# Kernel tuning notes

Measured on AMD Instinct MI355X. Metric: run time of the kernel, lower is better.

Reference implementation:

```python
import jax, jax.numpy as jnp
import numpy as np

HIDDEN, NH, NKV, HD = 2048, 16, 2, 128
CTX, NL, POS = 4096, 36, 3000
THETA, EPS = 1.0e6, 1e-6


def _rope_cos_sin(pos):
    inv_freq = 1.0 / (THETA ** (jnp.arange(0, HD, 2, dtype=jnp.float32) / HD))  # [HD/2]
    ang = pos * inv_freq
    ang = jnp.concatenate([ang, ang])  # [HD]
    return jnp.cos(ang), jnp.sin(ang)


def _rotate_half(x):
    x1, x2 = x[..., : HD // 2], x[..., HD // 2 :]
    return jnp.concatenate([-x2, x1], axis=-1)


def setup_inputs() -> dict:
    key = jax.random.key(0)
    ks = jax.random.split(key, 12)
    w = lambda k, shape, s=0.02: (jax.random.normal(k, shape, dtype=jnp.float32) * s)
    mask = jnp.where(jnp.arange(CTX) <= POS, 0.0, -1e9).astype(jnp.float32).reshape(1, 1, 1, CTX)
    return {
        "hidden_states": jax.random.normal(ks[0], (1, 1, HIDDEN), dtype=jnp.float32),
        "position_ids": jnp.array([POS], dtype=jnp.int64 if jax.config.jax_enable_x64 else jnp.int32),
        "causal_mask": mask,
        "current_pos": POS,
        "ln_w": jnp.ones((HIDDEN,), jnp.float32) + w(ks[1], (HIDDEN,)),
        "wq": w(ks[2], (NH * HD, HIDDEN)),
        "bq": w(ks[3], (NH * HD,)),
        "wk": w(ks[4], (NKV * HD, HIDDEN)),
        "bk": w(ks[5], (NKV * HD,)),
        "wv": w(ks[6], (NKV * HD, HIDDEN)),
        "bv": w(ks[7], (NKV * HD,)),
        "wo": w(ks[8], (HIDDEN, NH * HD)),
        "kv_cache": w(ks[9], (2 * NL, NKV, CTX, HD), 1.0),
    }


def reference(hidden_states, position_ids, causal_mask, current_pos,
              ln_w, wq, bq, wk, bk, wv, bv, wo, kv_cache):
    x = hidden_states  # [1,1,H]
    # RMSNorm
    var = jnp.mean(x * x, axis=-1, keepdims=True)
    nx = x * jax.lax.rsqrt(var + EPS) * ln_w

    # QKV projections (single token)
    t = nx[0, 0]  # [H]
    q = (wq @ t + bq).reshape(NH, HD)    # [NH, HD]
    k = (wk @ t + bk).reshape(NKV, HD)   # [NKV, HD]
    v = (wv @ t + bv).reshape(NKV, HD)

    # RoPE at current position
    cos, sin = _rope_cos_sin(jnp.float32(current_pos))
    q = q * cos + _rotate_half(q) * sin
    k = k * cos + _rotate_half(k) * sin

    # KV-cache scatter write: key at layer slot 0, value at slot NL
    kv_cache = kv_cache.at[0, :, current_pos, :].set(k)
    kv_cache = kv_cache.at[NL, :, current_pos, :].set(v)
    key_cache = kv_cache[0]    # [NKV, CTX, HD]
    value_cache = kv_cache[NL]

    # GQA attention over full cache
    rep = NH // NKV
    K = jnp.repeat(key_cache, rep, axis=0)    # [NH, CTX, HD]
    V = jnp.repeat(value_cache, rep, axis=0)
    scores = jnp.einsum("hd,hkd->hk", q, K) / jnp.sqrt(jnp.float32(HD))
    scores = scores + causal_mask[0, 0, 0]    # [NH, CTX]
    probs = jax.nn.softmax(scores, axis=-1)
    ctx = jnp.einsum("hk,hkd->hd", probs, V)  # [NH, HD]
    attn_out = (wo @ ctx.reshape(NH * HD)).reshape(1, 1, HIDDEN)

    return hidden_states + attn_out
```

## Files before the change

### kernel.cpp

```cpp
#include <hip/hip_runtime.h>
#include <hip/hip_bf16.h>
#include <math.h>

#define HIDDEN 2048
#define NH 16
#define NKV 2
#define HD 128
#define CTX 4096
#define NL 36
#define EPS 1e-6f

#define CHUNK 128
#define NCHUNKS (CTX / CHUNK)
#define HPB 4
#define NGRP (NH / HPB)

#define WS_QRAW 0
#define WS_KRAW 2048
#define WS_VRAW 2304
#define WS_TAB  2560
#define WS_PML  2688
#define WS_PACC 3712

#define RSQRT_HD 0.08838834764831845f

__device__ __forceinline__ float dot4(float4 a, float4 b) {
    return a.x*b.x + a.y*b.y + a.z*b.z + a.w*b.w;
}

__global__ __launch_bounds__(256, 1) void qkv_kernel(
    const float* __restrict__ x, const float* __restrict__ lnw,
    const float* __restrict__ wq, const float* __restrict__ bq,
    const float* __restrict__ wk, const float* __restrict__ bk,
    const float* __restrict__ wv, const float* __restrict__ bv,
    const int* __restrict__ curpos, float* __restrict__ ws)
{
    const int t = threadIdx.x;
    const int lane = t & 63, wid = t >> 6;

    if (blockIdx.x == 320) {
        if (t < 64) {
            double e = (double)t * (1.0 / 64.0);
            double invf = exp2(-19.931568569324174087 * e);
            double a = (double)curpos[0] * invf;
            a -= 6.2831853071795864769 * floor(a * 0.15915494309189533577);
            float s, c;
            sincosf((float)a, &s, &c);
            ws[WS_TAB + t] = c;
            ws[WS_TAB + 64 + t] = s;
        }
        return;
    }

    const int R0 = blockIdx.x * 8 + wid * 2;
    const float *w0, *w1; float b0, b1; float *dst0, *dst1;
    {
        int R = R0;
        if (R < 2048)      { w0 = wq + (size_t)R * HIDDEN;            b0 = bq[R];   dst0 = ws + WS_QRAW + R; }
        else if (R < 2304) { int r = R - 2048; w0 = wk + (size_t)r * HIDDEN; b0 = bk[r]; dst0 = ws + WS_KRAW + r; }
        else               { int r = R - 2304; w0 = wv + (size_t)r * HIDDEN; b0 = bv[r]; dst0 = ws + WS_VRAW + r; }
        R = R0 + 1;
        if (R < 2048)      { w1 = wq + (size_t)R * HIDDEN;            b1 = bq[R];   dst1 = ws + WS_QRAW + R; }
        else if (R < 2304) { int r = R - 2048; w1 = wk + (size_t)r * HIDDEN; b1 = bk[r]; dst1 = ws + WS_KRAW + r; }
        else               { int r = R - 2304; w1 = wv + (size_t)r * HIDDEN; b1 = bv[r]; dst1 = ws + WS_VRAW + r; }
    }
    const float4* w04 = (const float4*)w0;
    const float4* w14 = (const float4*)w1;
    float4 u[8], v[8];
    #pragma unroll
    for (int j = 0; j < 8; ++j) { u[j] = w04[j * 64 + lane]; v[j] = w14[j * 64 + lane]; }

    __shared__ float nx[HIDDEN];
    __shared__ float red[4];
    float4 xa = ((const float4*)x)[t * 2];
    float4 xb = ((const float4*)x)[t * 2 + 1];
    float ss = dot4(xa, xa) + dot4(xb, xb);
    #pragma unroll
    for (int m = 32; m; m >>= 1) ss += __shfl_xor(ss, m);
    if (lane == 0) red[wid] = ss;
    __syncthreads();
    float inv = rsqrtf((red[0] + red[1] + red[2] + red[3]) / (float)HIDDEN + EPS);
    float4 la = ((const float4*)lnw)[t * 2];
    float4 lb = ((const float4*)lnw)[t * 2 + 1];
    float4 na, nb;
    na.x = xa.x * inv * la.x; na.y = xa.y * inv * la.y;
    na.z = xa.z * inv * la.z; na.w = xa.w * inv * la.w;
    nb.x = xb.x * inv * lb.x; nb.y = xb.y * inv * lb.y;
    nb.z = xb.z * inv * lb.z; nb.w = xb.w * inv * lb.w;
    ((float4*)nx)[t * 2] = na;
    ((float4*)nx)[t * 2 + 1] = nb;
    __syncthreads();

    const float4* nx4 = (const float4*)nx;
    float a0 = 0.f, a1 = 0.f;
    #pragma unroll
    for (int j = 0; j < 8; ++j) {
        float4 n = nx4[j * 64 + lane];
        a0 += dot4(u[j], n);
        a1 += dot4(v[j], n);
    }
    #pragma unroll
    for (int m = 32; m; m >>= 1) { a0 += __shfl_xor(a0, m); a1 += __shfl_xor(a1, m); }
    if (lane == 0) { *dst0 = a0 + b0; *dst1 = a1 + b1; }
}

__global__ __launch_bounds__(256, 1) void attn_kernel(
    const float* __restrict__ kv, const int* __restrict__ curpos,
    float* __restrict__ ws)
{
    const int pos = curpos[0];
    const int grp = blockIdx.x / NCHUNKS;
    const int c = blockIdx.x % NCHUNKS;
    const int start = c * CHUNK;
    if (start > pos) return;
    const int nvalid = min(CHUNK, pos + 1 - start);
    const int h0 = grp * HPB;
    const int kvh = h0 / (NH / NKV);
    const float* kc = kv + (size_t)kvh * CTX * HD;
    const float* vc = kv + (size_t)(NL * NKV + kvh) * CTX * HD;

    __shared__ float tab[128];
    __shared__ float kf[HD];
    __shared__ float qr[HPB][HD];
    __shared__ float sc[HPB][CHUNK];
    __shared__ float ctxh[8][HPB][HD];

    const int t = threadIdx.x;
    const int lane = t & 63, wid = t >> 6;

    if (t < 128) tab[t] = ws[WS_TAB + t];
    __syncthreads();
    if (t < 128) {
        const float* kr = ws + WS_KRAW + (size_t)kvh * HD;
        float kvd = kr[t], kp = kr[t ^ 64];
        float r = (t < 64) ? -kp : kp;
        kf[t] = kvd * tab[t & 63] + r * tab[64 + (t & 63)];
    }
    #pragma unroll
    for (int i = 0; i < 2; ++i) {
        int e = t + i * 256;
        int hh = e >> 7, d = e & 127;
        const float* q = ws + WS_QRAW + (size_t)(h0 + hh) * HD;
        float qv = q[d], qp = q[d ^ 64];
        float r = (d < 64) ? -qp : qp;
        qr[hh][d] = (qv * tab[d & 63] + r * tab[64 + (d & 63)]) * RSQRT_HD;
    }
    __syncthreads();

    const int g16 = t >> 4, li = t & 15;
    float4 ka[8], kb[8];
    #pragma unroll
    for (int it = 0; it < 8; ++it) {
        const int p = start + it * 16 + g16;
        const float4* kp = (const float4*)(kc + (size_t)p * HD + li * 8);
        ka[it] = kp[0]; kb[it] = kp[1];
    }
    const int half = t >> 5, q4 = t & 31;
    float4 vv[16];
    #pragma unroll
    for (int i = 0; i < 16; ++i) {
        const int p = start + i * 8 + half;
        vv[i] = ((const float4*)(vc + (size_t)p * HD))[q4];
    }
    float4 fv = ((const float4*)(ws + WS_VRAW + (size_t)kvh * HD))[q4];

    float4 qa[HPB], qb[HPB];
    #pragma unroll
    for (int h = 0; h < HPB; ++h) {
        qa[h] = *(const float4*)&qr[h][li * 8];
        qb[h] = *(const float4*)&qr[h][li * 8 + 4];
    }

    #pragma unroll
    for (int it = 0; it < 8; ++it) {
        const int pl = it * 16 + g16;
        if (pl < nvalid) {
            float4 A = ka[it], B = kb[it];
            if (start + pl == pos) {
                A = *(const float4*)&kf[li * 8];
                B = *(const float4*)&kf[li * 8 + 4];
            }
            float s0 = dot4(qa[0], A) + dot4(qb[0], B);
            float s1 = dot4(qa[1], A) + dot4(qb[1], B);
            float s2 = dot4(qa[2], A) + dot4(qb[2], B);
            float s3 = dot4(qa[3], A) + dot4(qb[3], B);
            #pragma unroll
            for (int m = 1; m < 16; m <<= 1) {
                s0 += __shfl_xor(s0, m); s1 += __shfl_xor(s1, m);
                s2 += __shfl_xor(s2, m); s3 += __shfl_xor(s3, m);
            }
            if (li == 0) { sc[0][pl] = s0; sc[1][pl] = s1; sc[2][pl] = s2; sc[3][pl] = s3; }
        }
    }
    #pragma unroll
    for (int i = 0; i < 2; ++i) {
        int e = t + i * 256;
        int hh = e >> 7, pl = e & 127;
        if (pl >= nvalid) sc[hh][pl] = 0.f;
    }
    __syncthreads();

    {
        float m = -INFINITY;
        for (int p = lane; p < nvalid; p += 64) m = fmaxf(m, sc[wid][p]);
        #pragma unroll
        for (int mm = 32; mm; mm >>= 1) m = fmaxf(m, __shfl_xor(m, mm));
        float l = 0.f;
        for (int p = lane; p < nvalid; p += 64) {
            float e = expf(sc[wid][p] - m);
            sc[wid][p] = e;
            l += e;
        }
        #pragma unroll
        for (int mm = 32; mm; mm >>= 1) l += __shfl_xor(l, mm);
        if (lane == 0) {
            ws[WS_PML + ((size_t)(h0 + wid) * NCHUNKS + c) * 2]     = m;
            ws[WS_PML + ((size_t)(h0 + wid) * NCHUNKS + c) * 2 + 1] = l;
        }
    }
    __syncthreads();

    {
        float4 a[HPB];
        #pragma unroll
        for (int h = 0; h < HPB; ++h) a[h] = make_float4(0.f, 0.f, 0.f, 0.f);
        #pragma unroll
        for (int i = 0; i < 16; ++i) {
            const int pl = i * 8 + half;
            float4 x = (start + pl == pos) ? fv : vv[i];
            #pragma unroll
            for (int h = 0; h < HPB; ++h) {
                float w = sc[h][pl];
                a[h].x += w * x.x; a[h].y += w * x.y;
                a[h].z += w * x.z; a[h].w += w * x.w;
            }
        }
        #pragma unroll
        for (int h = 0; h < HPB; ++h)
            *(float4*)&ctxh[half][h][q4 * 4] = a[h];
    }
    __syncthreads();

    #pragma unroll
    for (int i = 0; i < 2; ++i) {
        int e = t + i * 256;
        int hh = e >> 7, d = e & 127;
        float s = 0.f;
        #pragma unroll
        for (int hf = 0; hf < 8; ++hf) s += ctxh[hf][hh][d];
        ws[WS_PACC + ((size_t)(h0 + hh) * NCHUNKS + c) * 128 + d] = s;
    }
}

__global__ __launch_bounds__(256, 1) void out_kernel(
    const float* __restrict__ wo, const float* __restrict__ hidden,
    const float* __restrict__ ws, const int* __restrict__ curpos,
    float* __restrict__ out)
{
    const int t = threadIdx.x;
    const int lane = t & 63, wid = t >> 6;

    const int row0 = blockIdx.x * 8 + wid * 2;
    const float4* w04 = (const float4*)(wo + (size_t)row0 * HIDDEN);
    const float4* w14 = (const float4*)(wo + (size_t)(row0 + 1) * HIDDEN);
    float4 u[8], v[8];
    #pragma unroll
    for (int j = 0; j < 8; ++j) { u[j] = w04[j * 64 + lane]; v[j] = w14[j * 64 + lane]; }

    __shared__ float ctx[HIDDEN];
    const int pos = curpos[0];
    const int nc = pos / CHUNK + 1;
    const int h = t >> 4, sub = t & 15;
    float M = -INFINITY;
    for (int c = 0; c < nc; ++c)
        M = fmaxf(M, ws[WS_PML + ((size_t)h * NCHUNKS + c) * 2]);
    float L = 0.f;
    float4 acc0 = make_float4(0.f,0.f,0.f,0.f), acc1 = make_float4(0.f,0.f,0.f,0.f);
    for (int c = 0; c < nc; ++c) {
        float mm = ws[WS_PML + ((size_t)h * NCHUNKS + c) * 2];
        float ll = ws[WS_PML + ((size_t)h * NCHUNKS + c) * 2 + 1];
        float w = expf(mm - M);
        L += w * ll;
        const float4* pa = (const float4*)(ws + WS_PACC + ((size_t)h * NCHUNKS + c) * 128 + sub * 8);
        float4 p0 = pa[0], p1 = pa[1];
        acc0.x += w*p0.x; acc0.y += w*p0.y; acc0.z += w*p0.z; acc0.w += w*p0.w;
        acc1.x += w*p1.x; acc1.y += w*p1.y; acc1.z += w*p1.z; acc1.w += w*p1.w;
    }
    float invL = 1.f / L;
    acc0.x *= invL; acc0.y *= invL; acc0.z *= invL; acc0.w *= invL;
    acc1.x *= invL; acc1.y *= invL; acc1.z *= invL; acc1.w *= invL;
    *(float4*)&ctx[h * HD + sub * 8]     = acc0;
    *(float4*)&ctx[h * HD + sub * 8 + 4] = acc1;
    __syncthreads();

    const float4* c4 = (const float4*)ctx;
    float a0 = 0.f, a1 = 0.f;
    #pragma unroll
    for (int j = 0; j < 8; ++j) {
        float4 n = c4[j * 64 + lane];
        a0 += dot4(u[j], n);
        a1 += dot4(v[j], n);
    }
    #pragma unroll
    for (int m = 32; m; m >>= 1) { a0 += __shfl_xor(a0, m); a1 += __shfl_xor(a1, m); }
    if (lane == 0) {
        out[row0]     = hidden[row0]     + a0;
        out[row0 + 1] = hidden[row0 + 1] + a1;
    }
}

extern "C" void kernel_launch(void* const* d_in, const int* in_sizes, int n_in,
                              void* d_out, int out_size, void* d_ws, size_t ws_size,
                              hipStream_t stream)
{
    const float* hidden = (const float*)d_in[0];
    const int*   cur    = (const int*)d_in[3];
    const float* lnw    = (const float*)d_in[4];
    const float* wq     = (const float*)d_in[5];
    const float* bq     = (const float*)d_in[6];
    const float* wk     = (const float*)d_in[7];
    const float* bk     = (const float*)d_in[8];
    const float* wv     = (const float*)d_in[9];
    const float* bv     = (const float*)d_in[10];
    const float* wo     = (const float*)d_in[11];
    const float* kv     = (const float*)d_in[12];
    float* ws  = (float*)d_ws;
    float* out = (float*)d_out;

    qkv_kernel<<<dim3(321), dim3(256), 0, stream>>>(hidden, lnw, wq, bq, wk, bk, wv, bv, cur, ws);
    attn_kernel<<<dim3(NGRP * NCHUNKS), dim3(256), 0, stream>>>(kv, cur, ws);
    out_kernel<<<dim3(256), dim3(256), 0, stream>>>(wo, hidden, ws, cur, out);
}
```

Baseline: 39.41 us.

## Fuse QKV, attention and output projection into one persistent kernel with grid barriers

Replaces the three kernel launches with a single 256-block persistent kernel that uses atomic-counter grid barriers between phases: QKV projection, chunked attention (8 heads per block sharing one KV head, so each KV chunk is read once), cross-chunk softmax merge, and output projection. The Wo weights are prefetched into registers before the barrier so the load overlaps the attention phase. RoPE table computation moves into the attention blocks, and a tiny init kernel resets the barrier counters. The aim is to remove launch gaps and halve KV re-reads. The cost is spin-wait barriers that depend on all 256 blocks being co-resident, higher register pressure, and idle blocks during attention.

```diff
diff --git a/kernel.cpp b/kernel.cpp
--- a/kernel.cpp
+++ b/kernel.cpp
@@ -11,16 +11,16 @@
 #define EPS 1e-6f
 
 #define CHUNK 128
-#define NCHUNKS (CTX / CHUNK)
-#define HPB 4
-#define NGRP (NH / HPB)
-
-#define WS_QRAW 0
-#define WS_KRAW 2048
-#define WS_VRAW 2304
-#define WS_TAB  2560
-#define WS_PML  2688
-#define WS_PACC 3712
+#define NCHUNKS 32
+#define HPB 8
+#define NGRP 2
+#define NBLK 256
+
+#define WS_QKV  0
+#define WS_PML  2560
+#define WS_PACC 3584
+#define WS_CTX  69120
+#define WS_SYNC 71168
 
 #define RSQRT_HD 0.08838834764831845f
 
@@ -28,272 +28,279 @@
     return a.x*b.x + a.y*b.y + a.z*b.z + a.w*b.w;
 }
 
-__global__ __launch_bounds__(256, 1) void qkv_kernel(
+__global__ void init_sync(float* __restrict__ ws) {
+    int* s = (int*)(ws + WS_SYNC);
+    if (threadIdx.x < 8) s[threadIdx.x] = 0;
+}
+
+__device__ __forceinline__ void gridbar(int* cnt, int t) {
+    __syncthreads();
+    if (t == 0) {
+        __hip_atomic_fetch_add(cnt, 1, __ATOMIC_ACQ_REL, __HIP_MEMORY_SCOPE_AGENT);
+        while (__hip_atomic_load(cnt, __ATOMIC_ACQUIRE, __HIP_MEMORY_SCOPE_AGENT) < NBLK)
+            __builtin_amdgcn_s_sleep(2);
+    }
+    __syncthreads();
+}
+
+__global__ __launch_bounds__(256, 2) void fused_kernel(
     const float* __restrict__ x, const float* __restrict__ lnw,
     const float* __restrict__ wq, const float* __restrict__ bq,
     const float* __restrict__ wk, const float* __restrict__ bk,
     const float* __restrict__ wv, const float* __restrict__ bv,
-    const int* __restrict__ curpos, float* __restrict__ ws)
+    const float* __restrict__ wo, const float* __restrict__ kvc,
+    const int* __restrict__ curpos, const float* __restrict__ hidden,
+    float* __restrict__ ws, float* __restrict__ out)
 {
     const int t = threadIdx.x;
     const int lane = t & 63, wid = t >> 6;
-
-    if (blockIdx.x == 320) {
-        if (t < 64) {
-            double e = (double)t * (1.0 / 64.0);
-            double invf = exp2(-19.931568569324174087 * e);
-            double a = (double)curpos[0] * invf;
-            a -= 6.2831853071795864769 * floor(a * 0.15915494309189533577);
-            float s, c;
-            sincosf((float)a, &s, &c);
-            ws[WS_TAB + t] = c;
-            ws[WS_TAB + 64 + t] = s;
-        }
-        return;
-    }
-
-    const int R0 = blockIdx.x * 8 + wid * 2;
-    const float *w0, *w1; float b0, b1; float *dst0, *dst1;
-    {
-        int R = R0;
-        if (R < 2048)      { w0 = wq + (size_t)R * HIDDEN;            b0 = bq[R];   dst0 = ws + WS_QRAW + R; }
-        else if (R < 2304) { int r = R - 2048; w0 = wk + (size_t)r * HIDDEN; b0 = bk[r]; dst0 = ws + WS_KRAW + r; }
-        else               { int r = R - 2304; w0 = wv + (size_t)r * HIDDEN; b0 = bv[r]; dst0 = ws + WS_VRAW + r; }
-        R = R0 + 1;
-        if (R < 2048)      { w1 = wq + (size_t)R * HIDDEN;            b1 = bq[R];   dst1 = ws + WS_QRAW + R; }
-        else if (R < 2304) { int r = R - 2048; w1 = wk + (size_t)r * HIDDEN; b1 = bk[r]; dst1 = ws + WS_KRAW + r; }
-        else               { int r = R - 2304; w1 = wv + (size_t)r * HIDDEN; b1 = bv[r]; dst1 = ws + WS_VRAW + r; }
-    }
-    const float4* w04 = (const float4*)w0;
-    const float4* w14 = (const float4*)w1;
-    float4 u[8], v[8];
-    #pragma unroll
-    for (int j = 0; j < 8; ++j) { u[j] = w04[j * 64 + lane]; v[j] = w14[j * 64 + lane]; }
-
-    __shared__ float nx[HIDDEN];
-    __shared__ float red[4];
-    float4 xa = ((const float4*)x)[t * 2];
-    float4 xb = ((const float4*)x)[t * 2 + 1];
-    float ss = dot4(xa, xa) + dot4(xb, xb);
-    #pragma unroll
-    for (int m = 32; m; m >>= 1) ss += __shfl_xor(ss, m);
-    if (lane == 0) red[wid] = ss;
-    __syncthreads();
-    float inv = rsqrtf((red[0] + red[1] + red[2] + red[3]) / (float)HIDDEN + EPS);
-    float4 la = ((const float4*)lnw)[t * 2];
-    float4 lb = ((const float4*)lnw)[t * 2 + 1];
-    float4 na, nb;
-    na.x = xa.x * inv * la.x; na.y = xa.y * inv * la.y;
-    na.z = xa.z * inv * la.z; na.w = xa.w * inv * la.w;
-    nb.x = xb.x * inv * lb.x; nb.y = xb.y * inv * lb.y;
-    nb.z = xb.z * inv * lb.z; nb.w = xb.w * inv * lb.w;
-    ((float4*)nx)[t * 2] = na;
-    ((float4*)nx)[t * 2 + 1] = nb;
-    __syncthreads();
-
-    const float4* nx4 = (const float4*)nx;
-    float a0 = 0.f, a1 = 0.f;
-    #pragma unroll
-    for (int j = 0; j < 8; ++j) {
-        float4 n = nx4[j * 64 + lane];
-        a0 += dot4(u[j], n);
-        a1 += dot4(v[j], n);
-    }
-    #pragma unroll
-    for (int m = 32; m; m >>= 1) { a0 += __shfl_xor(a0, m); a1 += __shfl_xor(a1, m); }
-    if (lane == 0) { *dst0 = a0 + b0; *dst1 = a1 + b1; }
-}
-
-__global__ __launch_bounds__(256, 1) void attn_kernel(
-    const float* __restrict__ kv, const int* __restrict__ curpos,
-    float* __restrict__ ws)
-{
+    const int b = blockIdx.x;
+    int* cnt = (int*)(ws + WS_SYNC);
     const int pos = curpos[0];
-    const int grp = blockIdx.x / NCHUNKS;
-    const int c = blockIdx.x % NCHUNKS;
-    const int start = c * CHUNK;
-    if (start > pos) return;
-    const int nvalid = min(CHUNK, pos + 1 - start);
-    const int h0 = grp * HPB;
-    const int kvh = h0 / (NH / NKV);
-    const float* kc = kv + (size_t)kvh * CTX * HD;
-    const float* vc = kv + (size_t)(NL * NKV + kvh) * CTX * HD;
-
+
+    __shared__ float redS[4];
+    __shared__ float redR[4][10];
     __shared__ float tab[128];
     __shared__ float kf[HD];
     __shared__ float qr[HPB][HD];
     __shared__ float sc[HPB][CHUNK];
     __shared__ float ctxh[8][HPB][HD];
-
-    const int t = threadIdx.x;
-    const int lane = t & 63, wid = t >> 6;
-
-    if (t < 128) tab[t] = ws[WS_TAB + t];
-    __syncthreads();
-    if (t < 128) {
-        const float* kr = ws + WS_KRAW + (size_t)kvh * HD;
-        float kvd = kr[t], kp = kr[t ^ 64];
-        float r = (t < 64) ? -kp : kp;
-        kf[t] = kvd * tab[t & 63] + r * tab[64 + (t & 63)];
-    }
-    #pragma unroll
-    for (int i = 0; i < 2; ++i) {
-        int e = t + i * 256;
-        int hh = e >> 7, d = e & 127;
-        const float* q = ws + WS_QRAW + (size_t)(h0 + hh) * HD;
-        float qv = q[d], qp = q[d ^ 64];
-        float r = (d < 64) ? -qp : qp;
-        qr[hh][d] = (qv * tab[d & 63] + r * tab[64 + (d & 63)]) * RSQRT_HD;
-    }
-    __syncthreads();
-
-    const int g16 = t >> 4, li = t & 15;
-    float4 ka[8], kb[8];
-    #pragma unroll
-    for (int it = 0; it < 8; ++it) {
-        const int p = start + it * 16 + g16;
-        const float4* kp = (const float4*)(kc + (size_t)p * HD + li * 8);
-        ka[it] = kp[0]; kb[it] = kp[1];
-    }
-    const int half = t >> 5, q4 = t & 31;
-    float4 vv[16];
-    #pragma unroll
-    for (int i = 0; i < 16; ++i) {
-        const int p = start + i * 8 + half;
-        vv[i] = ((const float4*)(vc + (size_t)p * HD))[q4];
-    }
-    float4 fv = ((const float4*)(ws + WS_VRAW + (size_t)kvh * HD))[q4];
-
-    float4 qa[HPB], qb[HPB];
-    #pragma unroll
-    for (int h = 0; h < HPB; ++h) {
-        qa[h] = *(const float4*)&qr[h][li * 8];
-        qb[h] = *(const float4*)&qr[h][li * 8 + 4];
-    }
-
-    #pragma unroll
-    for (int it = 0; it < 8; ++it) {
-        const int pl = it * 16 + g16;
-        if (pl < nvalid) {
-            float4 A = ka[it], B = kb[it];
-            if (start + pl == pos) {
-                A = *(const float4*)&kf[li * 8];
-                B = *(const float4*)&kf[li * 8 + 4];
-            }
-            float s0 = dot4(qa[0], A) + dot4(qb[0], B);
-            float s1 = dot4(qa[1], A) + dot4(qb[1], B);
-            float s2 = dot4(qa[2], A) + dot4(qb[2], B);
-            float s3 = dot4(qa[3], A) + dot4(qb[3], B);
-            #pragma unroll
-            for (int m = 1; m < 16; m <<= 1) {
-                s0 += __shfl_xor(s0, m); s1 += __shfl_xor(s1, m);
-                s2 += __shfl_xor(s2, m); s3 += __shfl_xor(s3, m);
-            }
-            if (li == 0) { sc[0][pl] = s0; sc[1][pl] = s1; sc[2][pl] = s2; sc[3][pl] = s3; }
-        }
-    }
-    #pragma unroll
-    for (int i = 0; i < 2; ++i) {
-        int e = t + i * 256;
-        int hh = e >> 7, pl = e & 127;
-        if (pl >= nvalid) sc[hh][pl] = 0.f;
-    }
-    __syncthreads();
-
-    {
-        float m = -INFINITY;
-        for (int p = lane; p < nvalid; p += 64) m = fmaxf(m, sc[wid][p]);
-        #pragma unroll
-        for (int mm = 32; mm; mm >>= 1) m = fmaxf(m, __shfl_xor(m, mm));
-        float l = 0.f;
-        for (int p = lane; p < nvalid; p += 64) {
-            float e = expf(sc[wid][p] - m);
-            sc[wid][p] = e;
-            l += e;
-        }
-        #pragma unroll
-        for (int mm = 32; mm; mm >>= 1) l += __shfl_xor(l, mm);
-        if (lane == 0) {
-            ws[WS_PML + ((size_t)(h0 + wid) * NCHUNKS + c) * 2]     = m;
-            ws[WS_PML + ((size_t)(h0 + wid) * NCHUNKS + c) * 2 + 1] = l;
-        }
-    }
-    __syncthreads();
-
-    {
-        float4 a[HPB];
-        #pragma unroll
-        for (int h = 0; h < HPB; ++h) a[h] = make_float4(0.f, 0.f, 0.f, 0.f);
+    __shared__ float ctx2[HIDDEN];
+
+    float4 qw0[10], qw1[10];
+    #pragma unroll
+    for (int r = 0; r < 10; ++r) {
+        const int R = b * 10 + r;
+        const float* w;
+        if (R < 2048)      w = wq + (size_t)R * HIDDEN;
+        else if (R < 2304) w = wk + (size_t)(R - 2048) * HIDDEN;
+        else               w = wv + (size_t)(R - 2304) * HIDDEN;
+        qw0[r] = ((const float4*)w)[t * 2];
+        qw1[r] = ((const float4*)w)[t * 2 + 1];
+    }
+
+    float4 xa = ((const float4*)x)[t * 2];
+    float4 xb = ((const float4*)x)[t * 2 + 1];
+    float ss = dot4(xa, xa) + dot4(xb, xb);
+    #pragma unroll
+    for (int m = 32; m; m >>= 1) ss += __shfl_xor(ss, m);
+    if (lane == 0) redS[wid] = ss;
+    __syncthreads();
+    const float inv = rsqrtf((redS[0] + redS[1] + redS[2] + redS[3]) * (1.f / HIDDEN) + EPS);
+    float4 la = ((const float4*)lnw)[t * 2];
+    float4 lb = ((const float4*)lnw)[t * 2 + 1];
+    float4 nxa, nxb;
+    nxa.x = xa.x * inv * la.x; nxa.y = xa.y * inv * la.y;
+    nxa.z = xa.z * inv * la.z; nxa.w = xa.w * inv * la.w;
+    nxb.x = xb.x * inv * lb.x; nxb.y = xb.y * inv * lb.y;
+    nxb.z = xb.z * inv * lb.z; nxb.w = xb.w * inv * lb.w;
+
+    float p[10];
+    #pragma unroll
+    for (int r = 0; r < 10; ++r)
+        p[r] = dot4(qw0[r], nxa) + dot4(qw1[r], nxb);
+    #pragma unroll
+    for (int r = 0; r < 10; ++r)
+        #pragma unroll
+        for (int m = 32; m; m >>= 1) p[r] += __shfl_xor(p[r], m);
+    if (lane == 0)
+        #pragma unroll
+        for (int r = 0; r < 10; ++r) redR[wid][r] = p[r];
+    __syncthreads();
+    if (t < 10) {
+        const int R = b * 10 + t;
+        float bias;
+        if (R < 2048)      bias = bq[R];
+        else if (R < 2304) bias = bk[R - 2048];
+        else               bias = bv[R - 2304];
+        ws[R] = redR[0][t] + redR[1][t] + redR[2][t] + redR[3][t] + bias;
+    }
+
+    gridbar(cnt + 0, t);
+
+    bool attnRole = false;
+    int grp = 0, c = 0, start = 0, nvalid = 0;
+    if (b < NGRP * NCHUNKS) {
+        grp = b >> 5; c = b & 31; start = c * CHUNK;
+        if (start <= pos) { attnRole = true; nvalid = min(CHUNK, pos + 1 - start); }
+    }
+
+    if (attnRole) {
+        const int h0 = grp * HPB, kvh = grp;
+        const float* kc = kvc + (size_t)kvh * CTX * HD;
+        const float* vc = kvc + (size_t)(NL * NKV + kvh) * CTX * HD;
+
+        if (t < 64) {
+            double e = (double)t * (1.0 / 64.0);
+            double invf = exp2(-19.931568569324174087 * e);
+            double a = (double)pos * invf;
+            a -= 6.2831853071795864769 * floor(a * 0.15915494309189533577);
+            float s, cs;
+            sincosf((float)a, &s, &cs);
+            tab[t] = cs; tab[64 + t] = s;
+        }
+        __syncthreads();
+        if (t < 128) {
+            const float* kr = ws + 2048 + (size_t)kvh * HD;
+            float kvd = kr[t], kp = kr[t ^ 64];
+            float r = (t < 64) ? -kp : kp;
+            kf[t] = kvd * tab[t & 63] + r * tab[64 + (t & 63)];
+        }
+        #pragma unroll
+        for (int i = 0; i < 4; ++i) {
+            int e = t + i * 256;
+            int hh = e >> 7, d = e & 127;
+            const float* q = ws + (size_t)(h0 + hh) * HD;
+            float qv = q[d], qp = q[d ^ 64];
+            float r = (d < 64) ? -qp : qp;
+            qr[hh][d] = (qv * tab[d & 63] + r * tab[64 + (d & 63)]) * RSQRT_HD;
+        }
+        __syncthreads();
+
+        const int g16 = t >> 4, li = t & 15;
+        float4 ka[8], kb[8];
+        #pragma unroll
+        for (int it = 0; it < 8; ++it) {
+            const int pp = start + it * 16 + g16;
+            const float4* kp = (const float4*)(kc + (size_t)pp * HD + li * 8);
+            ka[it] = kp[0]; kb[it] = kp[1];
+        }
+        const int half = t >> 5, q4 = t & 31;
+        float4 vv[16];
         #pragma unroll
         for (int i = 0; i < 16; ++i) {
-            const int pl = i * 8 + half;
-            float4 x = (start + pl == pos) ? fv : vv[i];
-            #pragma unroll
-            for (int h = 0; h < HPB; ++h) {
-                float w = sc[h][pl];
-                a[h].x += w * x.x; a[h].y += w * x.y;
-                a[h].z += w * x.z; a[h].w += w * x.w;
-            }
-        }
-        #pragma unroll
-        for (int h = 0; h < HPB; ++h)
-            *(float4*)&ctxh[half][h][q4 * 4] = a[h];
-    }
-    __syncthreads();
-
-    #pragma unroll
-    for (int i = 0; i < 2; ++i) {
-        int e = t + i * 256;
-        int hh = e >> 7, d = e & 127;
-        float s = 0.f;
-        #pragma unroll
-        for (int hf = 0; hf < 8; ++hf) s += ctxh[hf][hh][d];
-        ws[WS_PACC + ((size_t)(h0 + hh) * NCHUNKS + c) * 128 + d] = s;
-    }
-}
-
-__global__ __launch_bounds__(256, 1) void out_kernel(
-    const float* __restrict__ wo, const float* __restrict__ hidden,
-    const float* __restrict__ ws, const int* __restrict__ curpos,
-    float* __restrict__ out)
-{
-    const int t = threadIdx.x;
-    const int lane = t & 63, wid = t >> 6;
-
-    const int row0 = blockIdx.x * 8 + wid * 2;
+            const int pp = start + i * 8 + half;
+            vv[i] = ((const float4*)(vc + (size_t)pp * HD))[q4];
+        }
+        float4 fv = ((const float4*)(ws + 2304 + (size_t)kvh * HD))[q4];
+
+        #pragma unroll
+        for (int P = 0; P < 2; ++P) {
+            float4 qa[4], qb[4];
+            #pragma unroll
+            for (int hh = 0; hh < 4; ++hh) {
+                qa[hh] = *(const float4*)&qr[P * 4 + hh][li * 8];
+                qb[hh] = *(const float4*)&qr[P * 4 + hh][li * 8 + 4];
+            }
+            #pragma unroll
+            for (int it = 0; it < 8; ++it) {
+                const int pl = it * 16 + g16;
+                float4 A = ka[it], B = kb[it];
+                if (start + pl == pos) {
+                    A = *(const float4*)&kf[li * 8];
+                    B = *(const float4*)&kf[li * 8 + 4];
+                }
+                float s0 = dot4(qa[0], A) + dot4(qb[0], B);
+                float s1 = dot4(qa[1], A) + dot4(qb[1], B);
+                float s2 = dot4(qa[2], A) + dot4(qb[2], B);
+                float s3 = dot4(qa[3], A) + dot4(qb[3], B);
+                #pragma unroll
+                for (int m = 1; m < 16; m <<= 1) {
+                    s0 += __shfl_xor(s0, m); s1 += __shfl_xor(s1, m);
+                    s2 += __shfl_xor(s2, m); s3 += __shfl_xor(s3, m);
+                }
+                if (pl < nvalid && li == 0) {
+                    sc[P * 4 + 0][pl] = s0; sc[P * 4 + 1][pl] = s1;
+                    sc[P * 4 + 2][pl] = s2; sc[P * 4 + 3][pl] = s3;
+                }
+            }
+        }
+        #pragma unroll
+        for (int i = 0; i < 4; ++i) {
+            int e = t + i * 256;
+            int hh = e >> 7, pl = e & 127;
+            if (pl >= nvalid) sc[hh][pl] = 0.f;
+        }
+        __syncthreads();
+
+        #pragma unroll
+        for (int pass = 0; pass < 2; ++pass) {
+            const int hh = wid + pass * 4;
+            float m = -INFINITY;
+            for (int pp = lane; pp < nvalid; pp += 64) m = fmaxf(m, sc[hh][pp]);
+            #pragma unroll
+            for (int mm = 32; mm; mm >>= 1) m = fmaxf(m, __shfl_xor(m, mm));
+            float l = 0.f;
+            for (int pp = lane; pp < nvalid; pp += 64) {
+                float e = expf(sc[hh][pp] - m);
+                sc[hh][pp] = e;
+                l += e;
+            }
+            #pragma unroll
+            for (int mm = 32; mm; mm >>= 1) l += __shfl_xor(l, mm);
+            if (lane == 0) {
+                ws[WS_PML + ((size_t)(h0 + hh) * NCHUNKS + c) * 2]     = m;
+                ws[WS_PML + ((size_t)(h0 + hh) * NCHUNKS + c) * 2 + 1] = l;
+            }
+        }
+        __syncthreads();
+
+        #pragma unroll
+        for (int P = 0; P < 2; ++P) {
+            float4 a[4];
+            #pragma unroll
+            for (int hh = 0; hh < 4; ++hh) a[hh] = make_float4(0.f, 0.f, 0.f, 0.f);
+            #pragma unroll
+            for (int i = 0; i < 16; ++i) {
+                const int pl = i * 8 + half;
+                float4 xv = (start + pl == pos) ? fv : vv[i];
+                #pragma unroll
+                for (int hh = 0; hh < 4; ++hh) {
+                    float w = sc[P * 4 + hh][pl];
+                    a[hh].x += w * xv.x; a[hh].y += w * xv.y;
+                    a[hh].z += w * xv.z; a[hh].w += w * xv.w;
+                }
+            }
+            #pragma unroll
+            for (int hh = 0; hh < 4; ++hh)
+                *(float4*)&ctxh[half][P * 4 + hh][q4 * 4] = a[hh];
+        }
+        __syncthreads();
+
+        #pragma unroll
+        for (int i = 0; i < 4; ++i) {
+            int e = t + i * 256;
+            int hh = e >> 7, d = e & 127;
+            float s = 0.f;
+            #pragma unroll
+            for (int hf = 0; hf < 8; ++hf) s += ctxh[hf][hh][d];
+            ws[WS_PACC + ((size_t)(h0 + hh) * NCHUNKS + c) * 128 + d] = s;
+        }
+    }
+
+    const int row0 = b * 8 + wid * 2;
     const float4* w04 = (const float4*)(wo + (size_t)row0 * HIDDEN);
     const float4* w14 = (const float4*)(wo + (size_t)(row0 + 1) * HIDDEN);
     float4 u[8], v[8];
     #pragma unroll
     for (int j = 0; j < 8; ++j) { u[j] = w04[j * 64 + lane]; v[j] = w14[j * 64 + lane]; }
 
-    __shared__ float ctx[HIDDEN];
-    const int pos = curpos[0];
-    const int nc = pos / CHUNK + 1;
-    const int h = t >> 4, sub = t & 15;
-    float M = -INFINITY;
-    for (int c = 0; c < nc; ++c)
-        M = fmaxf(M, ws[WS_PML + ((size_t)h * NCHUNKS + c) * 2]);
-    float L = 0.f;
-    float4 acc0 = make_float4(0.f,0.f,0.f,0.f), acc1 = make_float4(0.f,0.f,0.f,0.f);
-    for (int c = 0; c < nc; ++c) {
-        float mm = ws[WS_PML + ((size_t)h * NCHUNKS + c) * 2];
-        float ll = ws[WS_PML + ((size_t)h * NCHUNKS + c) * 2 + 1];
-        float w = expf(mm - M);
-        L += w * ll;
-        const float4* pa = (const float4*)(ws + WS_PACC + ((size_t)h * NCHUNKS + c) * 128 + sub * 8);
-        float4 p0 = pa[0], p1 = pa[1];
-        acc0.x += w*p0.x; acc0.y += w*p0.y; acc0.z += w*p0.z; acc0.w += w*p0.w;
-        acc1.x += w*p1.x; acc1.y += w*p1.y; acc1.z += w*p1.z; acc1.w += w*p1.w;
-    }
-    float invL = 1.f / L;
-    acc0.x *= invL; acc0.y *= invL; acc0.z *= invL; acc0.w *= invL;
-    acc1.x *= invL; acc1.y *= invL; acc1.z *= invL; acc1.w *= invL;
-    *(float4*)&ctx[h * HD + sub * 8]     = acc0;
-    *(float4*)&ctx[h * HD + sub * 8 + 4] = acc1;
-    __syncthreads();
-
-    const float4* c4 = (const float4*)ctx;
+    gridbar(cnt + 1, t);
+
+    if (b < NH && t < 128) {
+        const int h = b;
+        const int nc = pos / CHUNK + 1;
+        float M = -INFINITY;
+        for (int c2 = 0; c2 < nc; ++c2)
+            M = fmaxf(M, ws[WS_PML + ((size_t)h * NCHUNKS + c2) * 2]);
+        float L = 0.f, acc = 0.f;
+        for (int c2 = 0; c2 < nc; ++c2) {
+            float mm = ws[WS_PML + ((size_t)h * NCHUNKS + c2) * 2];
+            float ll = ws[WS_PML + ((size_t)h * NCHUNKS + c2) * 2 + 1];
+            float w = expf(mm - M);
+            L += w * ll;
+            acc += w * ws[WS_PACC + ((size_t)h * NCHUNKS + c2) * 128 + t];
+        }
+        ws[WS_CTX + h * HD + t] = acc / L;
+    }
+
+    gridbar(cnt + 2, t);
+
+    ((float4*)ctx2)[t * 2]     = ((const float4*)(ws + WS_CTX))[t * 2];
+    ((float4*)ctx2)[t * 2 + 1] = ((const float4*)(ws + WS_CTX))[t * 2 + 1];
+    __syncthreads();
+
+    const float4* c4 = (const float4*)ctx2;
     float a0 = 0.f, a1 = 0.f;
     #pragma unroll
     for (int j = 0; j < 8; ++j) {
@@ -327,7 +334,7 @@
     float* ws  = (float*)d_ws;
     float* out = (float*)d_out;
 
-    qkv_kernel<<<dim3(321), dim3(256), 0, stream>>>(hidden, lnw, wq, bq, wk, bk, wv, bv, cur, ws);
-    attn_kernel<<<dim3(NGRP * NCHUNKS), dim3(256), 0, stream>>>(kv, cur, ws);
-    out_kernel<<<dim3(256), dim3(256), 0, stream>>>(wo, hidden, ws, cur, out);
-}
+    init_sync<<<dim3(1), dim3(64), 0, stream>>>(ws);
+    fused_kernel<<<dim3(NBLK), dim3(256), 0, stream>>>(
+        hidden, lnw, wq, bq, wk, bk, wv, bv, wo, kv, cur, hidden, ws, out);
+}
```

Result: slower. 140.2 us (+255.8%).

## Halve attention chunk size, compute RoPE table inside attention, prefetch KV earlier

Applied to the files above, without the earlier changes.

Attention chunks shrink from 128 to 64 positions, doubling the number of attention blocks to 256 so more CUs share the KV-cache read. Each block holds fewer K/V registers and uses single-pass softmax loops. The RoPE cos/sin table moves from a dedicated qkv block into each attention block, computed after the K/V loads are issued so the math overlaps memory latency. The cost is redundant sincos work per block and twice as many partial results for the out kernel to merge.

```diff
diff --git a/kernel.cpp b/kernel.cpp
--- a/kernel.cpp
+++ b/kernel.cpp
@@ -10,17 +10,17 @@
 #define NL 36
 #define EPS 1e-6f
 
-#define CHUNK 128
-#define NCHUNKS (CTX / CHUNK)
+#define CHUNK 64
+#define NCHUNKS 64
 #define HPB 4
-#define NGRP (NH / HPB)
+#define NGRP 4
+#define NATT 256
 
 #define WS_QRAW 0
 #define WS_KRAW 2048
 #define WS_VRAW 2304
-#define WS_TAB  2560
-#define WS_PML  2688
-#define WS_PACC 3712
+#define WS_PML  2560
+#define WS_PACC 4608
 
 #define RSQRT_HD 0.08838834764831845f
 
@@ -33,24 +33,10 @@
     const float* __restrict__ wq, const float* __restrict__ bq,
     const float* __restrict__ wk, const float* __restrict__ bk,
     const float* __restrict__ wv, const float* __restrict__ bv,
-    const int* __restrict__ curpos, float* __restrict__ ws)
+    float* __restrict__ ws)
 {
     const int t = threadIdx.x;
     const int lane = t & 63, wid = t >> 6;
-
-    if (blockIdx.x == 320) {
-        if (t < 64) {
-            double e = (double)t * (1.0 / 64.0);
-            double invf = exp2(-19.931568569324174087 * e);
-            double a = (double)curpos[0] * invf;
-            a -= 6.2831853071795864769 * floor(a * 0.15915494309189533577);
-            float s, c;
-            sincosf((float)a, &s, &c);
-            ws[WS_TAB + t] = c;
-            ws[WS_TAB + 64 + t] = s;
-        }
-        return;
-    }
 
     const int R0 = blockIdx.x * 8 + wid * 2;
     const float *w0, *w1; float b0, b1; float *dst0, *dst1;
@@ -79,7 +65,7 @@
     for (int m = 32; m; m >>= 1) ss += __shfl_xor(ss, m);
     if (lane == 0) red[wid] = ss;
     __syncthreads();
-    float inv = rsqrtf((red[0] + red[1] + red[2] + red[3]) / (float)HIDDEN + EPS);
+    float inv = rsqrtf((red[0] + red[1] + red[2] + red[3]) * (1.f / HIDDEN) + EPS);
     float4 la = ((const float4*)lnw)[t * 2];
     float4 lb = ((const float4*)lnw)[t * 2 + 1];
     float4 na, nb;
@@ -105,19 +91,19 @@
 }
 
 __global__ __launch_bounds__(256, 1) void attn_kernel(
-    const float* __restrict__ kv, const int* __restrict__ curpos,
+    const float* __restrict__ kvc, const int* __restrict__ curpos,
     float* __restrict__ ws)
 {
     const int pos = curpos[0];
-    const int grp = blockIdx.x / NCHUNKS;
-    const int c = blockIdx.x % NCHUNKS;
+    const int grp = blockIdx.x >> 6;
+    const int c = blockIdx.x & 63;
     const int start = c * CHUNK;
     if (start > pos) return;
     const int nvalid = min(CHUNK, pos + 1 - start);
     const int h0 = grp * HPB;
-    const int kvh = h0 / (NH / NKV);
-    const float* kc = kv + (size_t)kvh * CTX * HD;
-    const float* vc = kv + (size_t)(NL * NKV + kvh) * CTX * HD;
+    const int kvh = grp >> 1;
+    const float* kc = kvc + (size_t)kvh * CTX * HD;
+    const float* vc = kvc + (size_t)(NL * NKV + kvh) * CTX * HD;
 
     __shared__ float tab[128];
     __shared__ float kf[HD];
@@ -127,54 +113,72 @@
 
     const int t = threadIdx.x;
     const int lane = t & 63, wid = t >> 6;
-
-    if (t < 128) tab[t] = ws[WS_TAB + t];
-    __syncthreads();
+    const int g16 = t >> 4, li = t & 15;
+    const int half = t >> 5, q4 = t & 31;
+
+    float krv = 0.f, krp = 0.f;
     if (t < 128) {
         const float* kr = ws + WS_KRAW + (size_t)kvh * HD;
-        float kvd = kr[t], kp = kr[t ^ 64];
-        float r = (t < 64) ? -kp : kp;
-        kf[t] = kvd * tab[t & 63] + r * tab[64 + (t & 63)];
-    }
+        krv = kr[t]; krp = kr[t ^ 64];
+    }
+    float qv[2], qp[2];
     #pragma unroll
     for (int i = 0; i < 2; ++i) {
         int e = t + i * 256;
         int hh = e >> 7, d = e & 127;
         const float* q = ws + WS_QRAW + (size_t)(h0 + hh) * HD;
-        float qv = q[d], qp = q[d ^ 64];
-        float r = (d < 64) ? -qp : qp;
-        qr[hh][d] = (qv * tab[d & 63] + r * tab[64 + (d & 63)]) * RSQRT_HD;
-    }
-    __syncthreads();
-
-    const int g16 = t >> 4, li = t & 15;
-    float4 ka[8], kb[8];
-    #pragma unroll
-    for (int it = 0; it < 8; ++it) {
-        const int p = start + it * 16 + g16;
-        const float4* kp = (const float4*)(kc + (size_t)p * HD + li * 8);
+        qv[i] = q[d]; qp[i] = q[d ^ 64];
+    }
+    float4 fv = ((const float4*)(ws + WS_VRAW + (size_t)kvh * HD))[q4];
+
+    float4 ka[4], kb[4];
+    #pragma unroll
+    for (int it = 0; it < 4; ++it) {
+        const int pp = start + it * 16 + g16;
+        const float4* kp = (const float4*)(kc + (size_t)pp * HD + li * 8);
         ka[it] = kp[0]; kb[it] = kp[1];
     }
-    const int half = t >> 5, q4 = t & 31;
-    float4 vv[16];
-    #pragma unroll
-    for (int i = 0; i < 16; ++i) {
-        const int p = start + i * 8 + half;
-        vv[i] = ((const float4*)(vc + (size_t)p * HD))[q4];
-    }
-    float4 fv = ((const float4*)(ws + WS_VRAW + (size_t)kvh * HD))[q4];
-
-    float4 qa[HPB], qb[HPB];
-    #pragma unroll
-    for (int h = 0; h < HPB; ++h) {
-        qa[h] = *(const float4*)&qr[h][li * 8];
-        qb[h] = *(const float4*)&qr[h][li * 8 + 4];
-    }
-
-    #pragma unroll
-    for (int it = 0; it < 8; ++it) {
-        const int pl = it * 16 + g16;
-        if (pl < nvalid) {
+    float4 vv[8];
+    #pragma unroll
+    for (int i = 0; i < 8; ++i) {
+        const int pp = start + i * 8 + half;
+        vv[i] = ((const float4*)(vc + (size_t)pp * HD))[q4];
+    }
+
+    if (t < 64) {
+        double e = (double)t * (1.0 / 64.0);
+        double invf = exp2(-19.931568569324174087 * e);
+        double a = (double)pos * invf;
+        a -= 6.2831853071795864769 * floor(a * 0.15915494309189533577);
+        float s, cs;
+        sincosf((float)a, &s, &cs);
+        tab[t] = cs; tab[64 + t] = s;
+    }
+    __syncthreads();
+
+    if (t < 128) {
+        float r = (t < 64) ? -krp : krp;
+        kf[t] = krv * tab[t & 63] + r * tab[64 + (t & 63)];
+    }
+    #pragma unroll
+    for (int i = 0; i < 2; ++i) {
+        int e = t + i * 256;
+        int hh = e >> 7, d = e & 127;
+        float r = (d < 64) ? -qp[i] : qp[i];
+        qr[hh][d] = (qv[i] * tab[d & 63] + r * tab[64 + (d & 63)]) * RSQRT_HD;
+    }
+    __syncthreads();
+
+    {
+        float4 qa[4], qb[4];
+        #pragma unroll
+        for (int hh = 0; hh < 4; ++hh) {
+            qa[hh] = *(const float4*)&qr[hh][li * 8];
+            qb[hh] = *(const float4*)&qr[hh][li * 8 + 4];
+        }
+        #pragma unroll
+        for (int it = 0; it < 4; ++it) {
+            const int pl = it * 16 + g16;
             float4 A = ka[it], B = kb[it];
             if (start + pl == pos) {
                 A = *(const float4*)&kf[li * 8];
@@ -189,27 +193,25 @@
                 s0 += __shfl_xor(s0, m); s1 += __shfl_xor(s1, m);
                 s2 += __shfl_xor(s2, m); s3 += __shfl_xor(s3, m);
             }
-            if (li == 0) { sc[0][pl] = s0; sc[1][pl] = s1; sc[2][pl] = s2; sc[3][pl] = s3; }
-        }
-    }
-    #pragma unroll
-    for (int i = 0; i < 2; ++i) {
-        int e = t + i * 256;
-        int hh = e >> 7, pl = e & 127;
+            if (pl < nvalid && li == 0) {
+                sc[0][pl] = s0; sc[1][pl] = s1; sc[2][pl] = s2; sc[3][pl] = s3;
+            }
+        }
+    }
+    {
+        int hh = t >> 6, pl = t & 63;
         if (pl >= nvalid) sc[hh][pl] = 0.f;
     }
     __syncthreads();
 
     {
-        float m = -INFINITY;
-        for (int p = lane; p < nvalid; p += 64) m = fmaxf(m, sc[wid][p]);
+        float m = (lane < nvalid) ? sc[wid][lane] : -INFINITY;
         #pragma unroll
         for (int mm = 32; mm; mm >>= 1) m = fmaxf(m, __shfl_xor(m, mm));
         float l = 0.f;
-        for (int p = lane; p < nvalid; p += 64) {
-            float e = expf(sc[wid][p] - m);
-            sc[wid][p] = e;
-            l += e;
+        if (lane < nvalid) {
+            l = expf(sc[wid][lane] - m);
+            sc[wid][lane] = l;
         }
         #pragma unroll
         for (int mm = 32; mm; mm >>= 1) l += __shfl_xor(l, mm);
@@ -221,23 +223,23 @@
     __syncthreads();
 
     {
-        float4 a[HPB];
-        #pragma unroll
-        for (int h = 0; h < HPB; ++h) a[h] = make_float4(0.f, 0.f, 0.f, 0.f);
-        #pragma unroll
-        for (int i = 0; i < 16; ++i) {
+        float4 a[4];
+        #pragma unroll
+        for (int hh = 0; hh < 4; ++hh) a[hh] = make_float4(0.f, 0.f, 0.f, 0.f);
+        #pragma unroll
+        for (int i = 0; i < 8; ++i) {
             const int pl = i * 8 + half;
-            float4 x = (start + pl == pos) ? fv : vv[i];
+            float4 xv = (start + pl == pos) ? fv : vv[i];
             #pragma unroll
-            for (int h = 0; h < HPB; ++h) {
-                float w = sc[h][pl];
-                a[h].x += w * x.x; a[h].y += w * x.y;
-                a[h].z += w * x.z; a[h].w += w * x.w;
+            for (int hh = 0; hh < 4; ++hh) {
+                float w = sc[hh][pl];
+                a[hh].x += w * xv.x; a[hh].y += w * xv.y;
+                a[hh].z += w * xv.z; a[hh].w += w * xv.w;
             }
         }
         #pragma unroll
-        for (int h = 0; h < HPB; ++h)
-            *(float4*)&ctxh[half][h][q4 * 4] = a[h];
+        for (int hh = 0; hh < 4; ++hh)
+            *(float4*)&ctxh[half][hh][q4 * 4] = a[hh];
     }
     __syncthreads();
 
@@ -272,16 +274,16 @@
     const int nc = pos / CHUNK + 1;
     const int h = t >> 4, sub = t & 15;
     float M = -INFINITY;
-    for (int c = 0; c < nc; ++c)
-        M = fmaxf(M, ws[WS_PML + ((size_t)h * NCHUNKS + c) * 2]);
+    for (int c2 = 0; c2 < nc; ++c2)
+        M = fmaxf(M, ws[WS_PML + ((size_t)h * NCHUNKS + c2) * 2]);
     float L = 0.f;
     float4 acc0 = make_float4(0.f,0.f,0.f,0.f), acc1 = make_float4(0.f,0.f,0.f,0.f);
-    for (int c = 0; c < nc; ++c) {
-        float mm = ws[WS_PML + ((size_t)h * NCHUNKS + c) * 2];
-        float ll = ws[WS_PML + ((size_t)h * NCHUNKS + c) * 2 + 1];
+    for (int c2 = 0; c2 < nc; ++c2) {
+        float mm = ws[WS_PML + ((size_t)h * NCHUNKS + c2) * 2];
+        float ll = ws[WS_PML + ((size_t)h * NCHUNKS + c2) * 2 + 1];
         float w = expf(mm - M);
         L += w * ll;
-        const float4* pa = (const float4*)(ws + WS_PACC + ((size_t)h * NCHUNKS + c) * 128 + sub * 8);
+        const float4* pa = (const float4*)(ws + WS_PACC + ((size_t)h * NCHUNKS + c2) * 128 + sub * 8);
         float4 p0 = pa[0], p1 = pa[1];
         acc0.x += w*p0.x; acc0.y += w*p0.y; acc0.z += w*p0.z; acc0.w += w*p0.w;
         acc1.x += w*p1.x; acc1.y += w*p1.y; acc1.z += w*p1.z; acc1.w += w*p1.w;
@@ -327,7 +329,7 @@
     float* ws  = (float*)d_ws;
     float* out = (float*)d_out;
 
-    qkv_kernel<<<dim3(321), dim3(256), 0, stream>>>(hidden, lnw, wq, bq, wk, bk, wv, bv, cur, ws);
-    attn_kernel<<<dim3(NGRP * NCHUNKS), dim3(256), 0, stream>>>(kv, cur, ws);
+    qkv_kernel<<<dim3(320), dim3(256), 0, stream>>>(hidden, lnw, wq, bq, wk, bk, wv, bv, ws);
+    attn_kernel<<<dim3(NATT), dim3(256), 0, stream>>>(kv, cur, ws);
     out_kernel<<<dim3(256), dim3(256), 0, stream>>>(wo, hidden, ws, cur, out);
 }
```

Result: slower. 45.50 us (+15.5%).
